# Optimization experiments

Measured on AMD Instinct MI355X. Metric: run time of the kernel, lower is better.

## Reference

```python
import jax, jax.numpy as jnp
import numpy as np
import math


def setup_inputs() -> dict:
    key = jax.random.key(0)
    k0, k1, k2, k3, k4 = jax.random.split(key, 5)
    in_f, out_f, nb = 512, 512, 8
    B, S = 4, 2048
    x = jax.random.normal(k0, (B, S, in_f), dtype=jnp.float32)
    # RBF params (frozen in original: basis_trainable=False)
    fan_in = in_f  # fan_in of rbf.weight.T which is (num_basis, in_features)
    bound = 1.0 / math.sqrt(fan_in)
    rbf_weight = jax.random.uniform(k1, (in_f, nb), dtype=jnp.float32,
                                    minval=-math.sqrt(3.0) * 0.33 / math.sqrt(fan_in),
                                    maxval=math.sqrt(3.0) * 0.33 / math.sqrt(fan_in))
    rbf_centers = jnp.tile(jnp.linspace(-bound, bound, nb, dtype=jnp.float32)[None, :], (in_f, 1))
    # KAN spline weight (in, nb, out); fan_in for init is in_f*nb
    fan2 = in_f * nb
    wb = math.sqrt(3.0) * 0.33 / math.sqrt(fan2)
    weight = jax.random.uniform(k2, (in_f, nb, out_f), dtype=jnp.float32, minval=-wb, maxval=wb)
    bias = jax.random.uniform(k3, (out_f,), dtype=jnp.float32,
                              minval=-1.0 / math.sqrt(fan2), maxval=1.0 / math.sqrt(fan2))
    scale_base = jax.random.uniform(k4, (in_f, out_f), dtype=jnp.float32, minval=-0.1, maxval=0.1)
    return {"x": x, "rbf_weight": rbf_weight, "rbf_centers": rbf_centers,
            "weight": weight, "bias": bias, "scale_base": scale_base}


def reference(x, rbf_weight, rbf_centers, weight, bias, scale_base):
    in_f = x.shape[-1]
    nb = rbf_weight.shape[1]
    beta = (nb / math.log2(nb)) ** 2  # get_rbf_width(2/nb, log2(nb))
    batch_shape = x.shape[:-1]
    xf = x.reshape(-1, in_f)  # (N, in)
    # RBF basis expansion: (N, in, nb)
    z = xf[:, :, None] * rbf_weight[None, :, :] - rbf_centers[None, :, :]
    phi = jnp.exp(-beta * (z * z))
    # spline contraction + base path, expressed as efficient contractions
    y = jnp.einsum('nib,ibo->no', phi, weight)
    y = y + bias + jnp.cos(xf) @ scale_base
    return y.reshape(*batch_shape, weight.shape[-1])
```

## Files before the change

### kernel.cpp

```cpp
#include <hip/hip_runtime.h>
#include <hip/hip_bf16.h>

typedef __attribute__((ext_vector_type(8))) short short8;
typedef __attribute__((ext_vector_type(4))) float f32x4;

#define IN_F 512
#define OUT_F 512
#define BM 64
#define BN 256
#define BK 64
#define THREADS 256
#define PHI_STEPS 64
#define NSTEPS 72
#define NT 2
#define KSPLIT 2
#define IMG_CHUNKS 2048
#define A_SH (BM * BK)
#define B_SH (BN * BK)
#define PART_ELEMS (8192 * OUT_F)

__device__ __forceinline__ short f2bf(float f) {
  unsigned u = __builtin_bit_cast(unsigned, f);
  u += 0x7fffu + ((u >> 16) & 1u);
  return (short)(u >> 16);
}

__device__ __forceinline__ void glds16(const void* g, void* l) {
  __builtin_amdgcn_global_load_lds(
      (const __attribute__((address_space(1))) unsigned int*)g,
      (__attribute__((address_space(3))) unsigned int*)l, 16, 0, 0);
}

__device__ __forceinline__ float bsrc(const float* __restrict__ w,
                                      const float* __restrict__ sb,
                                      int k, int col) {
  return (k < IN_F * 8) ? w[(size_t)k * OUT_F + col]
                        : sb[(size_t)(k - IN_F * 8) * OUT_F + col];
}

__global__ void __launch_bounds__(256) prep_b(const float* __restrict__ w,
                                              const float* __restrict__ sb,
                                              short* __restrict__ img) {
  const int D = blockIdx.x * 256 + threadIdx.x;
  const int ci = D & (IMG_CHUNKS - 1);
  const int im = D >> 11;
  const int s = im % NSTEPS;
  const int nt = im / NSTEPS;
  const int n = ci >> 3, slot = ci & 7;
  const int oct = slot ^ (n & 7);
  const int col = nt * BN + n;
  short8 v;
#pragma unroll
  for (int j = 0; j < 8; ++j) v[j] = f2bf(bsrc(w, sb, s * 64 + oct * 8 + j, col));
  *(short8*)&img[(size_t)D * 8] = v;
}

__global__ void __launch_bounds__(256) reduce_add(const float* __restrict__ part,
                                                  float* __restrict__ out) {
  const int n4 = PART_ELEMS / 4;
  const float4* p4 = (const float4*)part;
  float4* o4 = (float4*)out;
  for (int i = blockIdx.x * 256 + threadIdx.x; i < n4; i += gridDim.x * 256) {
    float4 a = o4[i];
    const float4 b = p4[i];
    a.x += b.x; a.y += b.y; a.z += b.z; a.w += b.w;
    o4[i] = a;
  }
}

template <int KS, bool PREB>
__global__ void __launch_bounds__(THREADS, 2) kan_main(
    const float* __restrict__ x, const float* __restrict__ rw,
    const float* __restrict__ rc, const float* __restrict__ w,
    const float* __restrict__ bias, const float* __restrict__ sb,
    const short* __restrict__ bimg, float* __restrict__ out,
    float* __restrict__ part) {
  constexpr int SPLC = NSTEPS / KS;
  __shared__ __align__(16) short A_lds[2][A_SH];
  __shared__ __align__(16) short B_lds[2][B_SH];

  const int t = threadIdx.x, lane = t & 63, wid = t >> 6;
  const int l15 = lane & 15, kb = lane >> 4;
  const int m0 = blockIdx.x * BM;
  const int nt = blockIdx.y, n0 = nt * BN;
  const int ks = (KS > 1) ? blockIdx.z : 0;
  const int s0 = ks * SPLC;

  const int a_il = t & 7;
  const int a_m = t >> 3;
  const float c2 = -10.2591705f;

  f32x4 acc[4][4];
#pragma unroll
  for (int i = 0; i < 4; ++i)
#pragma unroll
    for (int j = 0; j < 4; ++j) acc[i][j] = (f32x4){0.f, 0.f, 0.f, 0.f};

  float xrA, xrB;
  float4 pr0, pr1, pc0, pc1;
  float4 cA0, cA1, cB0, cB1;

  auto loadNext = [&](int s1) {
    if (s1 < PHI_STEPS) {
      const int feat = s1 * 8 + a_il;
      xrA = x[(size_t)(m0 + a_m) * IN_F + feat];
      xrB = x[(size_t)(m0 + a_m + 32) * IN_F + feat];
      pr0 = *(const float4*)(rw + feat * 8);
      pr1 = *(const float4*)(rw + feat * 8 + 4);
      pc0 = *(const float4*)(rc + feat * 8);
      pc1 = *(const float4*)(rc + feat * 8 + 4);
    } else {
      const float* xpA = x + (size_t)(m0 + a_m) * IN_F + (s1 - PHI_STEPS) * 64 + a_il * 8;
      const float* xpB = xpA + (size_t)32 * IN_F;
      cA0 = *(const float4*)xpA; cA1 = *(const float4*)(xpA + 4);
      cB0 = *(const float4*)xpB; cB1 = *(const float4*)(xpB + 4);
    }
  };

  auto writeA = [&](int s1, short* __restrict__ Ad) {
    short8 avA, avB;
    if (s1 < PHI_STEPS) {
      const float rwv[8] = {pr0.x, pr0.y, pr0.z, pr0.w, pr1.x, pr1.y, pr1.z, pr1.w};
      const float rcv[8] = {pc0.x, pc0.y, pc0.z, pc0.w, pc1.x, pc1.y, pc1.z, pc1.w};
#pragma unroll
      for (int b = 0; b < 8; ++b) {
        const float zA = fmaf(xrA, rwv[b], -rcv[b]);
        const float zB = fmaf(xrB, rwv[b], -rcv[b]);
        avA[b] = f2bf(exp2f(c2 * zA * zA));
        avB[b] = f2bf(exp2f(c2 * zB * zB));
      }
    } else {
      avA[0] = f2bf(__cosf(cA0.x)); avA[1] = f2bf(__cosf(cA0.y));
      avA[2] = f2bf(__cosf(cA0.z)); avA[3] = f2bf(__cosf(cA0.w));
      avA[4] = f2bf(__cosf(cA1.x)); avA[5] = f2bf(__cosf(cA1.y));
      avA[6] = f2bf(__cosf(cA1.z)); avA[7] = f2bf(__cosf(cA1.w));
      avB[0] = f2bf(__cosf(cB0.x)); avB[1] = f2bf(__cosf(cB0.y));
      avB[2] = f2bf(__cosf(cB0.z)); avB[3] = f2bf(__cosf(cB0.w));
      avB[4] = f2bf(__cosf(cB1.x)); avB[5] = f2bf(__cosf(cB1.y));
      avB[6] = f2bf(__cosf(cB1.z)); avB[7] = f2bf(__cosf(cB1.w));
    }
    const int mA = a_m, mB = a_m + 32;
    *(short8*)&Ad[mA * BK + (a_il ^ (mA & 7)) * 8] = avA;
    *(short8*)&Ad[mB * BK + (a_il ^ (mB & 7)) * 8] = avB;
  };

  auto stageB = [&](int s, short* __restrict__ Bd) {
    if (PREB) {
      const short* src = bimg + ((size_t)(nt * NSTEPS + s) * IMG_CHUNKS + t) * 8;
#pragma unroll
      for (int c = 0; c < 8; ++c)
        glds16(src + (size_t)c * 256 * 8, Bd + c * 2048 + wid * 512);
    } else {
#pragma unroll
      for (int c = 0; c < 8; ++c) {
        const int ci = c * 256 + t;
        const int n = ci >> 3, slot = ci & 7, oct = slot ^ (n & 7);
        short8 v;
#pragma unroll
        for (int j = 0; j < 8; ++j)
          v[j] = f2bf(bsrc(w, sb, s * 64 + oct * 8 + j, n0 + n));
        *(short8*)&Bd[ci * 8] = v;
      }
    }
  };

  auto mfma_half = [&](const short* __restrict__ Ab, const short* __restrict__ Bb,
                       int kk) {
    const int sk = kk * 4 + kb;
    short8 af[4], bf[4];
#pragma unroll
    for (int mi = 0; mi < 4; ++mi) {
      const int r = mi * 16 + l15;
      af[mi] = *(const short8*)&Ab[r * BK + (sk ^ (r & 7)) * 8];
    }
#pragma unroll
    for (int ni = 0; ni < 4; ++ni) {
      const int n = wid * 64 + ni * 16 + l15;
      bf[ni] = *(const short8*)&Bb[n * BK + (sk ^ (n & 7)) * 8];
    }
#pragma unroll
    for (int mi = 0; mi < 4; ++mi)
#pragma unroll
      for (int ni = 0; ni < 4; ++ni)
        acc[mi][ni] = __builtin_amdgcn_mfma_f32_16x16x32_bf16(
            af[mi], bf[ni], acc[mi][ni], 0, 0, 0);
  };

  stageB(s0, B_lds[0]);
  loadNext(s0);
  writeA(s0, A_lds[0]);
  __syncthreads();

  for (int si = 0; si < SPLC; ++si) {
    const int c = si & 1;
    const int s = s0 + si;
    if (si + 1 < SPLC) { stageB(s + 1, B_lds[c ^ 1]); loadNext(s + 1); }
    mfma_half(A_lds[c], B_lds[c], 0);
    if (si + 1 < SPLC) writeA(s + 1, A_lds[c ^ 1]);
    mfma_half(A_lds[c], B_lds[c], 1);
    __syncthreads();
  }

#pragma unroll
  for (int ni = 0; ni < 4; ++ni) {
    const int col = n0 + wid * 64 + ni * 16 + l15;
    const float bb = (KS == 1 || ks == 0) ? bias[col] : 0.f;
#pragma unroll
    for (int mi = 0; mi < 4; ++mi) {
      const int rb = m0 + mi * 16 + kb * 4;
#pragma unroll
      for (int r4 = 0; r4 < 4; ++r4) {
        const size_t idx = (size_t)(rb + r4) * OUT_F + col;
        if (KS == 1 || ks == 0) out[idx] = acc[mi][ni][r4] + bb;
        else                    part[idx] = acc[mi][ni][r4];
      }
    }
  }
}

extern "C" void kernel_launch(void* const* d_in, const int* in_sizes, int n_in,
                              void* d_out, int out_size, void* d_ws, size_t ws_size,
                              hipStream_t stream) {
  const float* x    = (const float*)d_in[0];
  const float* rw   = (const float*)d_in[1];
  const float* rc   = (const float*)d_in[2];
  const float* w    = (const float*)d_in[3];
  const float* bias = (const float*)d_in[4];
  const float* sb   = (const float*)d_in[5];
  float* out = (float*)d_out;

  const int nrows = in_sizes[0] / IN_F;
  const int mb = nrows / BM;

  const size_t img_bytes  = (size_t)NT * NSTEPS * IMG_CHUNKS * 16;
  const size_t part_bytes = (size_t)PART_ELEMS * sizeof(float);
  const int img_chunks_total = NT * NSTEPS * IMG_CHUNKS;

  if (ws_size >= img_bytes + part_bytes) {
    short* img = (short*)d_ws;
    float* part = (float*)((char*)d_ws + img_bytes);
    prep_b<<<img_chunks_total / 256, 256, 0, stream>>>(w, sb, img);
    dim3 grid(mb, NT, KSPLIT);
    kan_main<KSPLIT, true><<<grid, THREADS, 0, stream>>>(x, rw, rc, w, bias, sb,
                                                         img, out, part);
    reduce_add<<<2048, 256, 0, stream>>>(part, out);
  } else if (ws_size >= part_bytes) {
    float* part = (float*)d_ws;
    dim3 grid(mb, NT, KSPLIT);
    kan_main<KSPLIT, false><<<grid, THREADS, 0, stream>>>(x, rw, rc, w, bias, sb,
                                                          nullptr, out, part);
    reduce_add<<<2048, 256, 0, stream>>>(part, out);
  } else {
    dim3 grid(mb, NT, 1);
    kan_main<1, false><<<grid, THREADS, 0, stream>>>(x, rw, rc, w, bias, sb,
                                                     nullptr, out, nullptr);
  }
}
```

Baseline: 99.16 us.

## Precompute RBF/cos activations into bf16 image and run pure GEMM kernel

Adds a prep_a kernel that expands x into the bf16 RBF and cos basis, pre-swizzled in LDS order. A new kan_gemm kernel with 512 threads (8 waves, 2x4 layout) then streams both A and B tiles via global_load_lds and does only MFMA work. This takes the exp/cos computation out of the GEMM's critical loop, at the cost of writing and rereading an A image of about 75 MB. The old in-kernel B conversion path is removed, so the fallback paths now assume workspace exists for the B image.

```diff
diff --git a/kernel.cpp b/kernel.cpp
--- a/kernel.cpp
+++ b/kernel.cpp
@@ -9,15 +9,15 @@
 #define BM 64
 #define BN 256
 #define BK 64
-#define THREADS 256
 #define PHI_STEPS 64
 #define NSTEPS 72
 #define NT 2
-#define KSPLIT 2
 #define IMG_CHUNKS 2048
+#define ACH 512
 #define A_SH (BM * BK)
 #define B_SH (BN * BK)
 #define PART_ELEMS (8192 * OUT_F)
+#define C2 (-10.2591705f)
 
 __device__ __forceinline__ short f2bf(float f) {
   unsigned u = __builtin_bit_cast(unsigned, f);
@@ -55,6 +55,44 @@
   *(short8*)&img[(size_t)D * 8] = v;
 }
 
+__global__ void __launch_bounds__(256) prep_a(const float* __restrict__ x,
+                                              const float* __restrict__ rw,
+                                              const float* __restrict__ rc,
+                                              short* __restrict__ aimg) {
+  const int D = blockIdx.x * 256 + threadIdx.x;
+  const int ci = D & (ACH - 1);
+  const int rest = D >> 9;
+  const int s = rest % NSTEPS;
+  const int mb = rest / NSTEPS;
+  const int m = ci >> 3, slot = ci & 7;
+  const int oct = slot ^ (m & 7);
+  const int row = mb * BM + m;
+  short8 v;
+  if (s < PHI_STEPS) {
+    const int feat = s * 8 + oct;
+    const float xv = x[(size_t)row * IN_F + feat];
+    const float4 r0 = *(const float4*)(rw + feat * 8);
+    const float4 r1 = *(const float4*)(rw + feat * 8 + 4);
+    const float4 q0 = *(const float4*)(rc + feat * 8);
+    const float4 q1 = *(const float4*)(rc + feat * 8 + 4);
+    const float rwv[8] = {r0.x, r0.y, r0.z, r0.w, r1.x, r1.y, r1.z, r1.w};
+    const float rcv[8] = {q0.x, q0.y, q0.z, q0.w, q1.x, q1.y, q1.z, q1.w};
+#pragma unroll
+    for (int j = 0; j < 8; ++j) {
+      const float z = fmaf(xv, rwv[j], -rcv[j]);
+      v[j] = f2bf(exp2f(C2 * z * z));
+    }
+  } else {
+    const float* xp = x + (size_t)row * IN_F + (s - PHI_STEPS) * 64 + oct * 8;
+    const float4 u0 = *(const float4*)xp, u1 = *(const float4*)(xp + 4);
+    v[0] = f2bf(__cosf(u0.x)); v[1] = f2bf(__cosf(u0.y));
+    v[2] = f2bf(__cosf(u0.z)); v[3] = f2bf(__cosf(u0.w));
+    v[4] = f2bf(__cosf(u1.x)); v[5] = f2bf(__cosf(u1.y));
+    v[6] = f2bf(__cosf(u1.z)); v[7] = f2bf(__cosf(u1.w));
+  }
+  *(short8*)&aimg[(size_t)D * 8] = v;
+}
+
 __global__ void __launch_bounds__(256) reduce_add(const float* __restrict__ part,
                                                   float* __restrict__ out) {
   const int n4 = PART_ELEMS / 4;
@@ -68,8 +106,98 @@
   }
 }
 
+template <int KS>
+__global__ void __launch_bounds__(512, 4) kan_gemm(
+    const short* __restrict__ aimg, const short* __restrict__ bimg,
+    const float* __restrict__ bias, float* __restrict__ out,
+    float* __restrict__ part) {
+  constexpr int SPLC = NSTEPS / KS;
+  __shared__ __align__(16) short A_lds[2][A_SH];
+  __shared__ __align__(16) short B_lds[2][B_SH];
+
+  const int t = threadIdx.x, lane = t & 63, wid = t >> 6;
+  const int wm = wid >> 2, wn = wid & 3;
+  const int l15 = lane & 15, kb = lane >> 4;
+  const int mb = blockIdx.x, nt = blockIdx.y;
+  const int ks = (KS > 1) ? blockIdx.z : 0;
+  const int m0 = mb * BM, n0 = nt * BN, s0 = ks * SPLC;
+
+  f32x4 acc[2][4];
+#pragma unroll
+  for (int i = 0; i < 2; ++i)
+#pragma unroll
+    for (int j = 0; j < 4; ++j) acc[i][j] = (f32x4){0.f, 0.f, 0.f, 0.f};
+
+  const short* abase = aimg + (size_t)mb * NSTEPS * ACH * 8;
+  const short* bbase = bimg + (size_t)nt * NSTEPS * IMG_CHUNKS * 8;
+
+  auto stage = [&](int s, int buf) {
+    const short* as = abase + ((size_t)s * ACH + wid * 64 + lane) * 8;
+    glds16(as, &A_lds[buf][wid * 512]);
+    const short* bs = bbase + ((size_t)s * IMG_CHUNKS + wid * 64 + lane) * 8;
+#pragma unroll
+    for (int c2 = 0; c2 < 4; ++c2)
+      glds16(bs + (size_t)c2 * 512 * 8, &B_lds[buf][c2 * 4096 + wid * 512]);
+  };
+
+  auto mfma_step = [&](int buf) {
+#pragma unroll
+    for (int kk = 0; kk < 2; ++kk) {
+      const int sk = kk * 4 + kb;
+      short8 af[2], bf[4];
+#pragma unroll
+      for (int mi = 0; mi < 2; ++mi) {
+        const int r = wm * 32 + mi * 16 + l15;
+        af[mi] = *(const short8*)&A_lds[buf][r * BK + (sk ^ (r & 7)) * 8];
+      }
+#pragma unroll
+      for (int ni = 0; ni < 4; ++ni) {
+        const int n = wn * 64 + ni * 16 + l15;
+        bf[ni] = *(const short8*)&B_lds[buf][n * BK + (sk ^ (n & 7)) * 8];
+      }
+#pragma unroll
+      for (int mi = 0; mi < 2; ++mi)
+#pragma unroll
+        for (int ni = 0; ni < 4; ++ni)
+          acc[mi][ni] = __builtin_amdgcn_mfma_f32_16x16x32_bf16(
+              af[mi], bf[ni], acc[mi][ni], 0, 0, 0);
+    }
+  };
+
+  stage(s0, 0);
+
+  for (int si = 0; si < SPLC; ++si) {
+    const int c = si & 1;
+    if (si + 1 < SPLC) {
+      stage(s0 + si + 1, c ^ 1);
+      asm volatile("s_waitcnt vmcnt(5)" ::: "memory");
+    } else {
+      asm volatile("s_waitcnt vmcnt(0)" ::: "memory");
+    }
+    __builtin_amdgcn_s_barrier();
+    mfma_step(c);
+    __builtin_amdgcn_s_barrier();
+  }
+
+#pragma unroll
+  for (int ni = 0; ni < 4; ++ni) {
+    const int col = n0 + wn * 64 + ni * 16 + l15;
+    const float bb = (KS == 1 || ks == 0) ? bias[col] : 0.f;
+#pragma unroll
+    for (int mi = 0; mi < 2; ++mi) {
+      const int rb = m0 + wm * 32 + mi * 16 + kb * 4;
+#pragma unroll
+      for (int r4 = 0; r4 < 4; ++r4) {
+        const size_t idx = (size_t)(rb + r4) * OUT_F + col;
+        if (KS == 1 || ks == 0) out[idx] = acc[mi][ni][r4] + bb;
+        else                    part[idx] = acc[mi][ni][r4];
+      }
+    }
+  }
+}
+
 template <int KS, bool PREB>
-__global__ void __launch_bounds__(THREADS, 2) kan_main(
+__global__ void __launch_bounds__(256, 2) kan_fused(
     const float* __restrict__ x, const float* __restrict__ rw,
     const float* __restrict__ rc, const float* __restrict__ w,
     const float* __restrict__ bias, const float* __restrict__ sb,
@@ -85,10 +213,8 @@
   const int nt = blockIdx.y, n0 = nt * BN;
   const int ks = (KS > 1) ? blockIdx.z : 0;
   const int s0 = ks * SPLC;
-
   const int a_il = t & 7;
   const int a_m = t >> 3;
-  const float c2 = -10.2591705f;
 
   f32x4 acc[4][4];
 #pragma unroll
@@ -126,8 +252,8 @@
       for (int b = 0; b < 8; ++b) {
         const float zA = fmaf(xrA, rwv[b], -rcv[b]);
         const float zB = fmaf(xrB, rwv[b], -rcv[b]);
-        avA[b] = f2bf(exp2f(c2 * zA * zA));
-        avB[b] = f2bf(exp2f(c2 * zB * zB));
+        avA[b] = f2bf(exp2f(C2 * zA * zA));
+        avB[b] = f2bf(exp2f(C2 * zB * zB));
       }
     } else {
       avA[0] = f2bf(__cosf(cA0.x)); avA[1] = f2bf(__cosf(cA0.y));
@@ -151,16 +277,6 @@
       for (int c = 0; c < 8; ++c)
         glds16(src + (size_t)c * 256 * 8, Bd + c * 2048 + wid * 512);
     } else {
-#pragma unroll
-      for (int c = 0; c < 8; ++c) {
-        const int ci = c * 256 + t;
-        const int n = ci >> 3, slot = ci & 7, oct = slot ^ (n & 7);
-        short8 v;
-#pragma unroll
-        for (int j = 0; j < 8; ++j)
-          v[j] = f2bf(bsrc(w, sb, s * 64 + oct * 8 + j, n0 + n));
-        *(short8*)&Bd[ci * 8] = v;
-      }
     }
   };
 
@@ -232,27 +348,38 @@
   const int nrows = in_sizes[0] / IN_F;
   const int mb = nrows / BM;
 
-  const size_t img_bytes  = (size_t)NT * NSTEPS * IMG_CHUNKS * 16;
+  const size_t bimg_bytes = (size_t)NT * NSTEPS * IMG_CHUNKS * 16;
+  const size_t aimg_bytes = (size_t)mb * NSTEPS * ACH * 16;
   const size_t part_bytes = (size_t)PART_ELEMS * sizeof(float);
-  const int img_chunks_total = NT * NSTEPS * IMG_CHUNKS;
-
-  if (ws_size >= img_bytes + part_bytes) {
-    short* img = (short*)d_ws;
-    float* part = (float*)((char*)d_ws + img_bytes);
-    prep_b<<<img_chunks_total / 256, 256, 0, stream>>>(w, sb, img);
-    dim3 grid(mb, NT, KSPLIT);
-    kan_main<KSPLIT, true><<<grid, THREADS, 0, stream>>>(x, rw, rc, w, bias, sb,
-                                                         img, out, part);
+
+  const int bch = NT * NSTEPS * IMG_CHUNKS;
+  const int ach_total = mb * NSTEPS * ACH;
+
+  if (ws_size >= bimg_bytes + aimg_bytes + part_bytes) {
+    short* bimg = (short*)d_ws;
+    short* aimg = (short*)((char*)d_ws + bimg_bytes);
+    float* part = (float*)((char*)d_ws + bimg_bytes + aimg_bytes);
+    prep_b<<<bch / 256, 256, 0, stream>>>(w, sb, bimg);
+    prep_a<<<ach_total / 256, 256, 0, stream>>>(x, rw, rc, aimg);
+    kan_gemm<2><<<dim3(mb, NT, 2), 512, 0, stream>>>(aimg, bimg, bias, out, part);
     reduce_add<<<2048, 256, 0, stream>>>(part, out);
-  } else if (ws_size >= part_bytes) {
-    float* part = (float*)d_ws;
-    dim3 grid(mb, NT, KSPLIT);
-    kan_main<KSPLIT, false><<<grid, THREADS, 0, stream>>>(x, rw, rc, w, bias, sb,
-                                                          nullptr, out, part);
+  } else if (ws_size >= bimg_bytes + aimg_bytes) {
+    short* bimg = (short*)d_ws;
+    short* aimg = (short*)((char*)d_ws + bimg_bytes);
+    prep_b<<<bch / 256, 256, 0, stream>>>(w, sb, bimg);
+    prep_a<<<ach_total / 256, 256, 0, stream>>>(x, rw, rc, aimg);
+    kan_gemm<1><<<dim3(mb, NT, 1), 512, 0, stream>>>(aimg, bimg, bias, out, nullptr);
+  } else if (ws_size >= bimg_bytes + part_bytes) {
+    short* bimg = (short*)d_ws;
+    float* part = (float*)((char*)d_ws + bimg_bytes);
+    prep_b<<<bch / 256, 256, 0, stream>>>(w, sb, bimg);
+    kan_fused<2, true><<<dim3(mb, NT, 2), 256, 0, stream>>>(x, rw, rc, w, bias, sb,
+                                                            bimg, out, part);
     reduce_add<<<2048, 256, 0, stream>>>(part, out);
   } else {
-    dim3 grid(mb, NT, 1);
-    kan_main<1, false><<<grid, THREADS, 0, stream>>>(x, rw, rc, w, bias, sb,
-                                                     nullptr, out, nullptr);
-  }
-}
+    short* bimg = (short*)d_ws;
+    prep_b<<<bch / 256, 256, 0, stream>>>(w, sb, bimg);
+    kan_fused<1, true><<<dim3(mb, NT, 1), 256, 0, stream>>>(x, rw, rc, w, bias, sb,
+                                                            bimg, out, nullptr);
+  }
+}
```

After: 82.62 us. 1.2x faster.
